# Performance work log

Hardware: AMD Instinct MI355X
Metric: run time of the kernel (lower is better)

Reference implementation:

```python
import jax, jax.numpy as jnp
import numpy as np

N = 50000
IN_CH = 256
HID = 256
E = 800000


def setup_inputs() -> dict:
    key = jax.random.key(0)
    ks = jax.random.split(key, 12)
    s = 1.0 / np.sqrt(HID)
    return {
        "x": jax.random.normal(ks[0], (N, IN_CH), jnp.float32),
        "edge_index": jax.random.randint(ks[1], (2, E), 0, N, dtype=jnp.int64),
        "prev_embedding": jax.random.normal(ks[2], (N, HID), jnp.float32),
        "W1": jax.random.normal(ks[3], (IN_CH, HID), jnp.float32) / np.sqrt(IN_CH),
        "b1": jnp.zeros((HID,), jnp.float32),
        "W2": jax.random.normal(ks[4], (HID, HID), jnp.float32) * s,
        "b2": jnp.zeros((HID,), jnp.float32),
        "gWw": jax.random.normal(ks[5], (HID, HID), jnp.float32) * s,
        "gWb": jnp.zeros((HID,), jnp.float32),
        "gUw": jax.random.normal(ks[6], (HID, HID), jnp.float32) * s,
        "gUb": jnp.zeros((HID,), jnp.float32),
    }


def _gcn_conv(x, W, b, src, dst, norm):
    # PyG GCNConv: h = x @ W; out[i] = sum_j norm_ij * h[j]; + bias
    h = x @ W
    msg = h[src] * norm[:, None]  # [E+N, H]
    out = jax.ops.segment_sum(msg, dst, num_segments=N)
    return out + b


def _norm_and_loops(edge_index):
    loop = jnp.arange(N, dtype=edge_index.dtype)
    src = jnp.concatenate([edge_index[0], loop])
    dst = jnp.concatenate([edge_index[1], loop])
    deg = jax.ops.segment_sum(jnp.ones_like(dst, dtype=jnp.float32), dst, num_segments=N)
    dinv = jnp.where(deg > 0, jax.lax.rsqrt(deg), 0.0)
    norm = dinv[src] * dinv[dst]
    return src, dst, norm


def reference(x, edge_index, prev_embedding, W1, b1, W2, b2, gWw, gWb, gUw, gUb):
    src, dst, norm = _norm_and_loops(edge_index)
    h = jax.nn.relu(_gcn_conv(x, W1, b1, src, dst, norm))
    h_t = _gcn_conv(h, W2, b2, src, dst, norm)
    alpha = jax.nn.sigmoid(h_t @ gWw + gWb + prev_embedding @ gUw + gUb)
    h_tilde = alpha * h_t + (1.0 - alpha) * prev_embedding
    return (h_tilde, h_t)
```

## Files before the change

### kernel.cpp

```cpp
#include <hip/hip_runtime.h>
#include <hip/hip_bf16.h>
#include <math.h>

#define HIDC 256
#define LSTR 56

typedef short short8 __attribute__((ext_vector_type(8)));
typedef float f32x4 __attribute__((ext_vector_type(4)));

__device__ __forceinline__ ushort f2bf_rne(float f) {
    uint u = __float_as_uint(f);
    u += 0x7FFF + ((u >> 16) & 1);
    return (ushort)(u >> 16);
}
__device__ __forceinline__ float bf2f(ushort h) {
    return __uint_as_float(((uint)h) << 16);
}


__global__ void fill_i_kernel(int* __restrict__ p, int v, int n) {
    int i = blockIdx.x * 256 + threadIdx.x;
    if (i < n) p[i] = v;
}

__global__ void deg_kernel(const int* __restrict__ dst, int* __restrict__ deg, int E) {
    int e = blockIdx.x * 256 + threadIdx.x;
    if (e < E) atomicAdd(&deg[dst[e]], 1);
}

__global__ void rsqrt_kernel(const int* __restrict__ deg, float* __restrict__ dinv, int n) {
    int i = blockIdx.x * 256 + threadIdx.x;
    if (i < n) dinv[i] = rsqrtf((float)(deg[i] + 1));
}


__device__ __forceinline__ int block_incl_scan(int v, int tid) {
#pragma unroll
    for (int off = 1; off < 64; off <<= 1) {
        int t = __shfl_up(v, off);
        if ((tid & 63) >= off) v += t;
    }
    __shared__ int wt[4];
    if ((tid & 63) == 63) wt[tid >> 6] = v;
    __syncthreads();
    int wid = tid >> 6;
    for (int w = 0; w < wid; w++) v += wt[w];
    __syncthreads();
    return v;
}

__global__ void scan_a_kernel(const int* __restrict__ deg, int* __restrict__ row_start,
                              int* __restrict__ blocksum, int N) {
    int tid = threadIdx.x;
    int i = blockIdx.x * 256 + tid;
    int v = (i < N) ? deg[i] : 0;
    int incl = block_incl_scan(v, tid);
    if (i < N) row_start[i + 1] = incl;
    if (tid == 255) blocksum[blockIdx.x] = incl;
}

__global__ void scan_b_kernel(int* __restrict__ blocksum, int nb) {
    int tid = threadIdx.x;
    int v = (tid < nb) ? blocksum[tid] : 0;
    int incl = block_incl_scan(v, tid);
    if (tid < nb) blocksum[tid] = incl;
}

__global__ void scan_c_kernel(int* __restrict__ row_start, int* __restrict__ cursor,
                              const int* __restrict__ blocksum, int N) {
    int b = blockIdx.x;
    int i = b * 256 + threadIdx.x;
    int add = (b > 0) ? blocksum[b - 1] : 0;
    if (i < N) {
        int v = row_start[i + 1] + add;
        row_start[i + 1] = v;
        cursor[i + 1] = v;
    }
    if (b == 0 && threadIdx.x == 0) { row_start[0] = 0; cursor[0] = 0; }
}

__global__ void scatter_kernel(const int* __restrict__ src, const int* __restrict__ dst,
                               const float* __restrict__ dinv, int* __restrict__ cursor,
                               int* __restrict__ csr_src, float* __restrict__ csr_w, int E) {
    int e = blockIdx.x * 256 + threadIdx.x;
    if (e < E) {
        int s = src[e], d = dst[e];
        int pos = atomicAdd(&cursor[d], 1);
        csr_src[pos] = s;
        csr_w[pos] = dinv[s] * dinv[d];
    }
}


__global__ void prep_bt_kernel(const float* __restrict__ B, ushort* __restrict__ Bt) {
    int n = blockIdx.x, k = threadIdx.x;
    Bt[n * 256 + k] = f2bf_rne(B[k * 256 + n]);
}

__global__ void prep_gate_bt_kernel(const float* __restrict__ gWw, const float* __restrict__ gUw,
                                    ushort* __restrict__ Bth, ushort* __restrict__ Btl) {
    int n = blockIdx.x, k = threadIdx.x;
    float v1 = gWw[k * 256 + n];
    uint u1 = __float_as_uint(v1);
    Bth[n * 512 + k] = (ushort)(u1 >> 16);
    Btl[n * 512 + k] = f2bf_rne(v1 - __uint_as_float(u1 & 0xFFFF0000u));
    float v2 = gUw[k * 256 + n];
    uint u2 = __float_as_uint(v2);
    Bth[n * 512 + 256 + k] = (ushort)(u2 >> 16);
    Btl[n * 512 + 256 + k] = f2bf_rne(v2 - __uint_as_float(u2 & 0xFFFF0000u));
}


__global__ __launch_bounds__(256) void gemm_bf16_kernel(
    const float* __restrict__ A, const ushort* __restrict__ Bt,
    ushort* __restrict__ C, int M)
{
    __shared__ __align__(16) ushort As[128 * LSTR];
    __shared__ __align__(16) ushort Bs[128 * LSTR];
    const int tl = threadIdx.x;
    const int lane = tl & 63, wave = tl >> 6;
    const int wm = (wave & 1) * 64, wn = (wave >> 1) * 64;
    const int bm = blockIdx.x * 128, bn = blockIdx.y * 128;

    const int ar  = tl >> 1;
    const int akq = (tl & 1) * 16;
    const bool aok = (bm + ar) < M;

    f32x4 acc[4][4] = {};

    for (int k0 = 0; k0 < 256; k0 += 32) {
        {
            const float* ap = A + (size_t)(bm + ar) * HIDC + k0 + akq;
#pragma unroll
            for (int j = 0; j < 4; j++) {
                float4 v = aok ? *(const float4*)(ap + 4 * j) : make_float4(0.f, 0.f, 0.f, 0.f);
                ushort4 h;
                h.x = f2bf_rne(v.x); h.y = f2bf_rne(v.y);
                h.z = f2bf_rne(v.z); h.w = f2bf_rne(v.w);
                *(ushort4*)&As[ar * LSTR + akq + 4 * j] = h;
            }
        }
        {
            const ushort* bp = Bt + (size_t)(bn + ar) * 256 + k0 + akq;
            *(uint4*)&Bs[ar * LSTR + akq]     = *(const uint4*)bp;
            *(uint4*)&Bs[ar * LSTR + akq + 8] = *(const uint4*)(bp + 8);
        }
        __syncthreads();
        const int fr = lane & 15, koff = (lane >> 4) * 8;
        short8 af[4], bfv[4];
#pragma unroll
        for (int t = 0; t < 4; t++) {
            af[t]  = *(const short8*)&As[(wm + t * 16 + fr) * LSTR + koff];
            bfv[t] = *(const short8*)&Bs[(wn + t * 16 + fr) * LSTR + koff];
        }
#pragma unroll
        for (int mt = 0; mt < 4; mt++)
#pragma unroll
            for (int nt = 0; nt < 4; nt++)
                acc[mt][nt] = __builtin_amdgcn_mfma_f32_16x16x32_bf16(af[mt], bfv[nt], acc[mt][nt], 0, 0, 0);
        __syncthreads();
    }

    const int row4 = (lane >> 4) * 4, coln = lane & 15;
#pragma unroll
    for (int mt = 0; mt < 4; mt++)
#pragma unroll
        for (int r = 0; r < 4; r++) {
            int m = bm + wm + mt * 16 + row4 + r;
            if (m < M) {
#pragma unroll
                for (int nt = 0; nt < 4; nt++) {
                    int n = bn + wn + nt * 16 + coln;
                    C[(size_t)m * HIDC + n] = f2bf_rne(acc[mt][nt][r]);
                }
            }
        }
}


__global__ __launch_bounds__(256) void gate_kernel(
    const float* __restrict__ ht, const float* __restrict__ prev,
    const ushort* __restrict__ Bth, const ushort* __restrict__ Btl,
    const float* __restrict__ gWb, const float* __restrict__ gUb,
    float* __restrict__ out, int M)
{
    __shared__ __align__(16) ushort Ash[128 * LSTR];
    __shared__ __align__(16) ushort Asl[128 * LSTR];
    __shared__ __align__(16) ushort Bsh[128 * LSTR];
    __shared__ __align__(16) ushort Bsl[128 * LSTR];
    const int tl = threadIdx.x;
    const int lane = tl & 63, wave = tl >> 6;
    const int wm = (wave & 1) * 64, wn = (wave >> 1) * 64;
    const int bm = blockIdx.x * 128, bn = blockIdx.y * 128;

    const int ar  = tl >> 1;
    const int akq = (tl & 1) * 16;
    const bool aok = (bm + ar) < M;

    f32x4 acc[4][4] = {};

    for (int k0 = 0; k0 < 512; k0 += 32) {
        {
            const float* srcA = (k0 < 256) ? ht : prev;
            const float* ap = srcA + (size_t)(bm + ar) * HIDC + (k0 & 255) + akq;
#pragma unroll
            for (int j = 0; j < 4; j++) {
                float4 v = aok ? *(const float4*)(ap + 4 * j) : make_float4(0.f, 0.f, 0.f, 0.f);
                float vv[4] = {v.x, v.y, v.z, v.w};
                ushort4 hh, ll;
                ushort* hp = (ushort*)&hh; ushort* lp = (ushort*)&ll;
#pragma unroll
                for (int q = 0; q < 4; q++) {
                    uint u = __float_as_uint(vv[q]);
                    hp[q] = (ushort)(u >> 16);
                    lp[q] = f2bf_rne(vv[q] - __uint_as_float(u & 0xFFFF0000u));
                }
                *(ushort4*)&Ash[ar * LSTR + akq + 4 * j] = hh;
                *(ushort4*)&Asl[ar * LSTR + akq + 4 * j] = ll;
            }
        }
        {
            const ushort* bph = Bth + (size_t)(bn + ar) * 512 + k0 + akq;
            const ushort* bpl = Btl + (size_t)(bn + ar) * 512 + k0 + akq;
            *(uint4*)&Bsh[ar * LSTR + akq]     = *(const uint4*)bph;
            *(uint4*)&Bsh[ar * LSTR + akq + 8] = *(const uint4*)(bph + 8);
            *(uint4*)&Bsl[ar * LSTR + akq]     = *(const uint4*)bpl;
            *(uint4*)&Bsl[ar * LSTR + akq + 8] = *(const uint4*)(bpl + 8);
        }
        __syncthreads();
        const int fr = lane & 15, koff = (lane >> 4) * 8;
        short8 afh[4], afl[4], bfh[4], bfl[4];
#pragma unroll
        for (int t = 0; t < 4; t++) {
            afh[t] = *(const short8*)&Ash[(wm + t * 16 + fr) * LSTR + koff];
            afl[t] = *(const short8*)&Asl[(wm + t * 16 + fr) * LSTR + koff];
            bfh[t] = *(const short8*)&Bsh[(wn + t * 16 + fr) * LSTR + koff];
            bfl[t] = *(const short8*)&Bsl[(wn + t * 16 + fr) * LSTR + koff];
        }
#pragma unroll
        for (int mt = 0; mt < 4; mt++)
#pragma unroll
            for (int nt = 0; nt < 4; nt++) {
                acc[mt][nt] = __builtin_amdgcn_mfma_f32_16x16x32_bf16(afh[mt], bfh[nt], acc[mt][nt], 0, 0, 0);
                acc[mt][nt] = __builtin_amdgcn_mfma_f32_16x16x32_bf16(afh[mt], bfl[nt], acc[mt][nt], 0, 0, 0);
                acc[mt][nt] = __builtin_amdgcn_mfma_f32_16x16x32_bf16(afl[mt], bfh[nt], acc[mt][nt], 0, 0, 0);
            }
        __syncthreads();
    }

    const int row4 = (lane >> 4) * 4, coln = lane & 15;
#pragma unroll
    for (int mt = 0; mt < 4; mt++)
#pragma unroll
        for (int r = 0; r < 4; r++) {
            int m = bm + wm + mt * 16 + row4 + r;
            if (m < M) {
#pragma unroll
                for (int nt = 0; nt < 4; nt++) {
                    int n = bn + wn + nt * 16 + coln;
                    size_t idx = (size_t)m * HIDC + n;
                    float g = acc[mt][nt][r] + gWb[n] + gUb[n];
                    float alpha = 1.f / (1.f + expf(-g));
                    out[idx] = alpha * ht[idx] + (1.f - alpha) * prev[idx];
                }
            }
        }
}


__global__ __launch_bounds__(256) void csr_agg_kernel(
    const ushort* __restrict__ hm, const int* __restrict__ row_start,
    const int* __restrict__ csr_src, const float* __restrict__ csr_w,
    const float* __restrict__ dinv, const float* __restrict__ bias,
    float* __restrict__ out, int do_relu) {
    __shared__ int   s_idx[64];
    __shared__ float s_w[64];
    const int i = blockIdx.x;
    const int c = threadIdx.x;
    const int b0 = row_start[i];
    const int b1 = row_start[i + 1];
    const float di = dinv[i];
    float acc = di * di * bf2f(hm[(size_t)i * HIDC + c]);
    for (int cb = b0; cb < b1; cb += 64) {
        int m = min(64, b1 - cb);
        if (c < m) {
            s_idx[c] = csr_src[cb + c];
            s_w[c]   = csr_w[cb + c];
        }
        __syncthreads();
        for (int t = 0; t < m; t++) {
            int s = s_idx[t];
            acc += s_w[t] * bf2f(hm[(size_t)s * HIDC + c]);
        }
        __syncthreads();
    }
    acc += bias[c];
    if (do_relu) acc = fmaxf(acc, 0.f);
    out[(size_t)i * HIDC + c] = acc;
}


extern "C" void kernel_launch(void* const* d_in, const int* in_sizes, int n_in,
                              void* d_out, int out_size, void* d_ws, size_t ws_size,
                              hipStream_t stream) {
    const float* x    = (const float*)d_in[0];
    const int*   ei   = (const int*)d_in[1];
    const float* prev = (const float*)d_in[2];
    const float* W1   = (const float*)d_in[3];
    const float* b1   = (const float*)d_in[4];
    const float* W2   = (const float*)d_in[5];
    const float* b2   = (const float*)d_in[6];
    const float* gWw  = (const float*)d_in[7];
    const float* gWb  = (const float*)d_in[8];
    const float* gUw  = (const float*)d_in[9];
    const float* gUb  = (const float*)d_in[10];

    const int N = in_sizes[0] / HIDC;
    const int E = in_sizes[1] / 2;
    const int* src = ei;
    const int* dst = ei + E;

    float* out  = (float*)d_out;
    float* out1 = out;
    float* ht   = out + (size_t)N * HIDC;

    float* ws = (float*)d_ws;
    size_t o = 0;
    auto take = [&](size_t n) { size_t r = o; o += (n + 63) & ~(size_t)63; return r; };
    float*  dinv    = ws + take(N);
    int*    degi    = (int*)(ws + take(N));
    int*    row_st  = (int*)(ws + take(N + 1));
    int*    cursor  = (int*)(ws + take(N + 1));
    int*    csr_src = (int*)(ws + take(E));
    float*  csr_w   = ws + take(E);
    ushort* Bt1     = (ushort*)(ws + take(256 * 256 / 2));
    ushort* Bt2     = (ushort*)(ws + take(256 * 256 / 2));
    ushort* Bth     = (ushort*)(ws + take(256 * 512 / 2));
    ushort* Btl     = (ushort*)(ws + take(256 * 512 / 2));
    ushort* hm      = (ushort*)(ws + take((size_t)N * HIDC / 2));

    const int nbN = (N + 255) / 256;
    const int nbE = (E + 255) / 256;
    dim3 ggrid((N + 127) / 128, 2);

    int* blocksum = (int*)csr_w;
    fill_i_kernel<<<nbN, 256, 0, stream>>>(degi, 0, N);
    deg_kernel<<<nbE, 256, 0, stream>>>(dst, degi, E);
    scan_a_kernel<<<nbN, 256, 0, stream>>>(degi, row_st, blocksum, N);
    scan_b_kernel<<<1, 256, 0, stream>>>(blocksum, nbN);
    scan_c_kernel<<<nbN, 256, 0, stream>>>(row_st, cursor, blocksum, N);
    rsqrt_kernel<<<nbN, 256, 0, stream>>>(degi, dinv, N);
    scatter_kernel<<<nbE, 256, 0, stream>>>(src, dst, dinv, cursor, csr_src, csr_w, E);

    prep_bt_kernel<<<256, 256, 0, stream>>>(W1, Bt1);
    prep_bt_kernel<<<256, 256, 0, stream>>>(W2, Bt2);
    prep_gate_bt_kernel<<<256, 256, 0, stream>>>(gWw, gUw, Bth, Btl);

    gemm_bf16_kernel<<<ggrid, 256, 0, stream>>>(x, Bt1, hm, N);
    csr_agg_kernel<<<N, 256, 0, stream>>>(hm, row_st, csr_src, csr_w, dinv, b1, out1, 1);

    gemm_bf16_kernel<<<ggrid, 256, 0, stream>>>(out1, Bt2, hm, N);
    csr_agg_kernel<<<N, 256, 0, stream>>>(hm, row_st, csr_src, csr_w, dinv, b2, ht, 0);

    gate_kernel<<<ggrid, 256, 0, stream>>>(ht, prev, Bth, Btl, gWb, gUb, out1, N);

    (void)n_in; (void)out_size; (void)ws_size;
}
```

Before: 611.5 us.

## Use wave-per-node vectorized CSR aggregation with bf16 intermediate and bf16-input GEMM

Rewrites the CSR aggregation so each wavefront handles one node, with each lane owning four channels. Edge indices and weights are read directly, without shared staging or block barriers, and the loop is unrolled by four to keep more gathers in flight. The first layer's aggregated output is now written as bf16 and consumed by a new GEMM variant that loads bf16 A directly, halving that intermediate's traffic and removing the fp32-to-bf16 conversion in the GEMM load. The change also shrinks the LDS row stride and adds an occupancy hint to launch_bounds. The smaller stride may raise LDS bank conflicts.

```diff
diff --git a/kernel.cpp b/kernel.cpp
--- a/kernel.cpp
+++ b/kernel.cpp
@@ -3,7 +3,7 @@
 #include <math.h>
 
 #define HIDC 256
-#define LSTR 56
+#define LSTR 40
 
 typedef short short8 __attribute__((ext_vector_type(8)));
 typedef float f32x4 __attribute__((ext_vector_type(4)));
@@ -111,7 +111,7 @@
 }
 
 
-__global__ __launch_bounds__(256) void gemm_bf16_kernel(
+__global__ __launch_bounds__(256, 4) void gemm_bf16_kernel(
     const float* __restrict__ A, const ushort* __restrict__ Bt,
     ushort* __restrict__ C, int M)
 {
@@ -178,7 +178,69 @@
 }
 
 
-__global__ __launch_bounds__(256) void gate_kernel(
+__global__ __launch_bounds__(256, 4) void gemm_bf16A_kernel(
+    const ushort* __restrict__ A, const ushort* __restrict__ Bt,
+    ushort* __restrict__ C, int M)
+{
+    __shared__ __align__(16) ushort As[128 * LSTR];
+    __shared__ __align__(16) ushort Bs[128 * LSTR];
+    const int tl = threadIdx.x;
+    const int lane = tl & 63, wave = tl >> 6;
+    const int wm = (wave & 1) * 64, wn = (wave >> 1) * 64;
+    const int bm = blockIdx.x * 128, bn = blockIdx.y * 128;
+
+    const int ar  = tl >> 1;
+    const int akq = (tl & 1) * 16;
+    const bool aok = (bm + ar) < M;
+
+    f32x4 acc[4][4] = {};
+
+    for (int k0 = 0; k0 < 256; k0 += 32) {
+        {
+            const ushort* ap = A + (size_t)(bm + ar) * HIDC + k0 + akq;
+            uint4 z = make_uint4(0u, 0u, 0u, 0u);
+            *(uint4*)&As[ar * LSTR + akq]     = aok ? *(const uint4*)ap       : z;
+            *(uint4*)&As[ar * LSTR + akq + 8] = aok ? *(const uint4*)(ap + 8) : z;
+        }
+        {
+            const ushort* bp = Bt + (size_t)(bn + ar) * 256 + k0 + akq;
+            *(uint4*)&Bs[ar * LSTR + akq]     = *(const uint4*)bp;
+            *(uint4*)&Bs[ar * LSTR + akq + 8] = *(const uint4*)(bp + 8);
+        }
+        __syncthreads();
+        const int fr = lane & 15, koff = (lane >> 4) * 8;
+        short8 af[4], bfv[4];
+#pragma unroll
+        for (int t = 0; t < 4; t++) {
+            af[t]  = *(const short8*)&As[(wm + t * 16 + fr) * LSTR + koff];
+            bfv[t] = *(const short8*)&Bs[(wn + t * 16 + fr) * LSTR + koff];
+        }
+#pragma unroll
+        for (int mt = 0; mt < 4; mt++)
+#pragma unroll
+            for (int nt = 0; nt < 4; nt++)
+                acc[mt][nt] = __builtin_amdgcn_mfma_f32_16x16x32_bf16(af[mt], bfv[nt], acc[mt][nt], 0, 0, 0);
+        __syncthreads();
+    }
+
+    const int row4 = (lane >> 4) * 4, coln = lane & 15;
+#pragma unroll
+    for (int mt = 0; mt < 4; mt++)
+#pragma unroll
+        for (int r = 0; r < 4; r++) {
+            int m = bm + wm + mt * 16 + row4 + r;
+            if (m < M) {
+#pragma unroll
+                for (int nt = 0; nt < 4; nt++) {
+                    int n = bn + wn + nt * 16 + coln;
+                    C[(size_t)m * HIDC + n] = f2bf_rne(acc[mt][nt][r]);
+                }
+            }
+        }
+}
+
+
+__global__ __launch_bounds__(256, 4) void gate_kernel(
     const float* __restrict__ ht, const float* __restrict__ prev,
     const ushort* __restrict__ Bth, const ushort* __restrict__ Btl,
     const float* __restrict__ gWb, const float* __restrict__ gUb,
@@ -272,31 +334,56 @@
     const ushort* __restrict__ hm, const int* __restrict__ row_start,
     const int* __restrict__ csr_src, const float* __restrict__ csr_w,
     const float* __restrict__ dinv, const float* __restrict__ bias,
-    float* __restrict__ out, int do_relu) {
-    __shared__ int   s_idx[64];
-    __shared__ float s_w[64];
-    const int i = blockIdx.x;
-    const int c = threadIdx.x;
-    const int b0 = row_start[i];
-    const int b1 = row_start[i + 1];
+    float* __restrict__ outf, ushort* __restrict__ outb, int do_relu, int N)
+{
+    const int wave = threadIdx.x >> 6, lane = threadIdx.x & 63;
+    const int i = blockIdx.x * 4 + wave;
+    if (i >= N) return;
+    const int c = lane * 4;
+
     const float di = dinv[i];
-    float acc = di * di * bf2f(hm[(size_t)i * HIDC + c]);
-    for (int cb = b0; cb < b1; cb += 64) {
-        int m = min(64, b1 - cb);
-        if (c < m) {
-            s_idx[c] = csr_src[cb + c];
-            s_w[c]   = csr_w[cb + c];
-        }
-        __syncthreads();
-        for (int t = 0; t < m; t++) {
-            int s = s_idx[t];
-            acc += s_w[t] * bf2f(hm[(size_t)s * HIDC + c]);
-        }
-        __syncthreads();
-    }
-    acc += bias[c];
-    if (do_relu) acc = fmaxf(acc, 0.f);
-    out[(size_t)i * HIDC + c] = acc;
+    const float s2 = di * di;
+    ushort4 sv = *(const ushort4*)(hm + (size_t)i * HIDC + c);
+    float a0 = s2 * bf2f(sv.x), a1 = s2 * bf2f(sv.y);
+    float a2 = s2 * bf2f(sv.z), a3 = s2 * bf2f(sv.w);
+
+    const int b0 = row_start[i], b1 = row_start[i + 1];
+    int t = b0;
+    for (; t + 4 <= b1; t += 4) {
+        int   i0 = csr_src[t],     i1 = csr_src[t + 1];
+        int   i2 = csr_src[t + 2], i3 = csr_src[t + 3];
+        float w0 = csr_w[t],       w1 = csr_w[t + 1];
+        float w2 = csr_w[t + 2],   w3 = csr_w[t + 3];
+        ushort4 v0 = *(const ushort4*)(hm + (size_t)i0 * HIDC + c);
+        ushort4 v1 = *(const ushort4*)(hm + (size_t)i1 * HIDC + c);
+        ushort4 v2 = *(const ushort4*)(hm + (size_t)i2 * HIDC + c);
+        ushort4 v3 = *(const ushort4*)(hm + (size_t)i3 * HIDC + c);
+        a0 += w0 * bf2f(v0.x); a1 += w0 * bf2f(v0.y); a2 += w0 * bf2f(v0.z); a3 += w0 * bf2f(v0.w);
+        a0 += w1 * bf2f(v1.x); a1 += w1 * bf2f(v1.y); a2 += w1 * bf2f(v1.z); a3 += w1 * bf2f(v1.w);
+        a0 += w2 * bf2f(v2.x); a1 += w2 * bf2f(v2.y); a2 += w2 * bf2f(v2.z); a3 += w2 * bf2f(v2.w);
+        a0 += w3 * bf2f(v3.x); a1 += w3 * bf2f(v3.y); a2 += w3 * bf2f(v3.z); a3 += w3 * bf2f(v3.w);
+    }
+    for (; t < b1; ++t) {
+        int s_ = csr_src[t];
+        float w = csr_w[t];
+        ushort4 v = *(const ushort4*)(hm + (size_t)s_ * HIDC + c);
+        a0 += w * bf2f(v.x); a1 += w * bf2f(v.y); a2 += w * bf2f(v.z); a3 += w * bf2f(v.w);
+    }
+
+    float4 bb = *(const float4*)(bias + c);
+    a0 += bb.x; a1 += bb.y; a2 += bb.z; a3 += bb.w;
+    if (do_relu) {
+        a0 = fmaxf(a0, 0.f); a1 = fmaxf(a1, 0.f);
+        a2 = fmaxf(a2, 0.f); a3 = fmaxf(a3, 0.f);
+    }
+    if (outb) {
+        ushort4 o;
+        o.x = f2bf_rne(a0); o.y = f2bf_rne(a1);
+        o.z = f2bf_rne(a2); o.w = f2bf_rne(a3);
+        *(ushort4*)(outb + (size_t)i * HIDC + c) = o;
+    } else {
+        *(float4*)(outf + (size_t)i * HIDC + c) = make_float4(a0, a1, a2, a3);
+    }
 }
 
 
@@ -323,6 +410,7 @@
     float* out  = (float*)d_out;
     float* out1 = out;
     float* ht   = out + (size_t)N * HIDC;
+    ushort* hbf = (ushort*)out1;
 
     float* ws = (float*)d_ws;
     size_t o = 0;
@@ -342,6 +430,7 @@
     const int nbN = (N + 255) / 256;
     const int nbE = (E + 255) / 256;
     dim3 ggrid((N + 127) / 128, 2);
+    const int nbAgg = (N + 3) / 4;
 
     int* blocksum = (int*)csr_w;
     fill_i_kernel<<<nbN, 256, 0, stream>>>(degi, 0, N);
@@ -357,10 +446,12 @@
     prep_gate_bt_kernel<<<256, 256, 0, stream>>>(gWw, gUw, Bth, Btl);
 
     gemm_bf16_kernel<<<ggrid, 256, 0, stream>>>(x, Bt1, hm, N);
-    csr_agg_kernel<<<N, 256, 0, stream>>>(hm, row_st, csr_src, csr_w, dinv, b1, out1, 1);
-
-    gemm_bf16_kernel<<<ggrid, 256, 0, stream>>>(out1, Bt2, hm, N);
-    csr_agg_kernel<<<N, 256, 0, stream>>>(hm, row_st, csr_src, csr_w, dinv, b2, ht, 0);
+    csr_agg_kernel<<<nbAgg, 256, 0, stream>>>(hm, row_st, csr_src, csr_w, dinv, b1,
+                                              nullptr, hbf, 1, N);
+
+    gemm_bf16A_kernel<<<ggrid, 256, 0, stream>>>(hbf, Bt2, hm, N);
+    csr_agg_kernel<<<nbAgg, 256, 0, stream>>>(hm, row_st, csr_src, csr_w, dinv, b2,
+                                              ht, nullptr, 0, N);
 
     gate_kernel<<<ggrid, 256, 0, stream>>>(ht, prev, Bth, Btl, gWb, gUb, out1, N);
 
```

Result: faster. 510.1 us (-16.6%).
